# Performance work log

Measured on AMD Instinct MI355X. Metric: run time of the kernel, lower is better.

The kernel has to match this reference:

```python
import jax, jax.numpy as jnp
import numpy as np

B, S, HID, H, DK = 16, 1024, 512, 8, 64
NEG = -1e30


def setup_inputs() -> dict:
    key = jax.random.key(0)
    kx, kl, kq, kk, kv, ko = jax.random.split(key, 6)
    x = jax.random.normal(kx, (B, S, HID), dtype=jnp.float32)
    # mask is a prefix of ones per sample (the torch code fills nmask[i, :nsum, :nsum])
    lengths = jax.random.randint(kl, (B,), S // 2, S + 1)
    mask = (jnp.arange(S)[None, :] < lengths[:, None]).astype(jnp.int32)
    scale = 0.02
    Wq = jax.random.normal(kq, (H, HID, DK), dtype=jnp.float32) * scale  # stacked per-head Linear weights
    Wk = jax.random.normal(kk, (H, HID, DK), dtype=jnp.float32) * scale
    Wv = jax.random.normal(kv, (H, HID, DK), dtype=jnp.float32) * scale
    Wout = jax.random.normal(ko, (H * DK, HID), dtype=jnp.float32) * scale
    return {"x": x, "mask": mask, "Wq": Wq, "Wk": Wk, "Wv": Wv, "Wout": Wout}


def reference(x, mask, Wq, Wk, Wv, Wout):
    # x: [B,S,HID], mask: [B,S] int prefix mask
    nsum = mask.sum(-1).astype(jnp.float32)          # [B]
    valid = mask.astype(bool)                         # [B,S]
    pair = valid[:, :, None] & valid[:, None, :]      # [B,S,S] == nmask from the torch loop
    # batched per-head projections (equivalent to the per-head Linear loop)
    Q = jnp.einsum('bsh,nhd->bnsd', x, Wq)            # [B,H,S,DK]
    K = jnp.einsum('bsh,nhd->bnsd', x, Wk)
    V = jnp.einsum('bsh,nhd->bnsd', x, Wv)
    scores = jnp.einsum('bnqd,bnkd->bnqk', Q, K)      # [B,H,S,S]
    scores = scores / jnp.sqrt(nsum)[:, None, None, None]  # per-sample sqrt(len) scale
    scores = jnp.where(pair[:, None, :, :], scores, NEG)   # masked_softmax: -1e30 at masked slots
    p = jax.nn.softmax(scores, axis=-1)
    attn = jnp.einsum('bnqk,bnkd->bnqd', p, V)        # [B,H,S,DK]
    h = attn.transpose(0, 2, 1, 3).reshape(B, S, H * DK)  # concat heads along feature dim
    return jnp.einsum('bsf,fh->bsh', h, Wout)         # W_out, no bias
```

## Files before the change

kernel.cpp:

```cpp
#include <hip/hip_runtime.h>
#include <math.h>

constexpr int CB = 16;
constexpr int CS = 1024;
constexpr int CHID = 512;
constexpr int CH = 8;
constexpr int CDK = 64;

typedef _Float16 f16;
typedef __attribute__((ext_vector_type(8))) _Float16 f16x8;
typedef __attribute__((ext_vector_type(4))) _Float16 f16x4;
typedef __attribute__((ext_vector_type(4))) float f32x4;

__device__ inline f32x4 mfma16(f16x8 a, f16x8 b, f32x4 c) {
  return __builtin_amdgcn_mfma_f32_16x16x32_f16(a, b, c, 0, 0, 0);
}

__global__ __launch_bounds__(256) void lengths_kernel(const int* __restrict__ mask,
                                                      int* __restrict__ lens) {
  const int b = blockIdx.x, t = threadIdx.x;
  __shared__ int red[256];
  int s = 0;
  for (int i = t; i < CS; i += 256) s += mask[b * CS + i];
  red[t] = s;
  __syncthreads();
  for (int off = 128; off > 0; off >>= 1) {
    if (t < off) red[t] += red[t + off];
    __syncthreads();
  }
  if (t == 0) lens[b] = red[0];
}

__global__ __launch_bounds__(256) void cast_x_kernel(const float4* __restrict__ x,
                                                     f16x4* __restrict__ xh) {
  const int idx = blockIdx.x * 256 + threadIdx.x;
  const float4 v = x[idx];
  f16x4 o;
  o[0] = (f16)v.x; o[1] = (f16)v.y; o[2] = (f16)v.z; o[3] = (f16)v.w;
  xh[idx] = o;
}

__global__ __launch_bounds__(256) void cast_w_kernel(const float* __restrict__ Wq,
                                                     const float* __restrict__ Wk,
                                                     const float* __restrict__ Wv,
                                                     const float* __restrict__ Wout,
                                                     f16* __restrict__ wtAll) {
  const int y = blockIdx.y;
  const int o0 = (blockIdx.x * 256 + threadIdx.x) * 4;
  f16* D = wtAll + (size_t)y * 262144;
  f16x4 d;
  if (y < 3) {
    const float* W = (y == 0) ? Wq : (y == 1) ? Wk : Wv;
    const int h = o0 >> 15, n = (o0 >> 9) & 63, k = o0 & 511;
    const size_t in = (size_t)h * 32768 + (size_t)k * 64 + n;
#pragma unroll
    for (int j = 0; j < 4; ++j) d[j] = (f16)W[in + (size_t)j * 64];
  } else {
    const int n = o0 >> 9, k = o0 & 511;
#pragma unroll
    for (int j = 0; j < 4; ++j) d[j] = (f16)Wout[(size_t)(k + j) * 512 + n];
  }
  *(f16x4*)&D[o0] = d;
}

__global__ __launch_bounds__(256) void qkvf_kernel(
    const f16* __restrict__ xh, const f16* __restrict__ wtAll,
    const int* __restrict__ lens, f16* __restrict__ Qh, f16* __restrict__ Kh,
    f16* __restrict__ Vth) {
  const int rt = blockIdx.x, ct = blockIdx.y;
  const int which = ct >> 2, hp = ct & 3;
  const f16* Wt = wtAll + (size_t)which * 262144 + (size_t)hp * 65536;
  const int row0 = rt * 128;
  const int b = row0 >> 10, s0 = row0 & 1023;
  const int h0 = hp * 2;
  const int t = threadIdx.x;
  const int w = t >> 6, lane = t & 63, quad = lane >> 4, lcol = lane & 15;
  const int wr = w >> 1, wc = w & 1;

  __shared__ union SM {
    struct { f16 Xs[128][40]; f16 Ws[128][40]; } a;
    f16 Ts[128][136];
  } sm;

  f32x4 acc[4][4];
#pragma unroll
  for (int i = 0; i < 4; ++i)
#pragma unroll
    for (int j = 0; j < 4; ++j) acc[i][j] = (f32x4){0.f, 0.f, 0.f, 0.f};

  for (int k0 = 0; k0 < CHID; k0 += 32) {
#pragma unroll
    for (int i = 0; i < 2; ++i) {
      const int c = t + 256 * i, r = c >> 2, sg = c & 3;
      *(f16x8*)&sm.a.Xs[r][sg * 8] =
          *(const f16x8*)&xh[(size_t)(row0 + r) * CHID + k0 + sg * 8];
      *(f16x8*)&sm.a.Ws[r][sg * 8] =
          *(const f16x8*)&Wt[(size_t)r * CHID + k0 + sg * 8];
    }
    __syncthreads();
    f16x8 af[4], bf[4];
#pragma unroll
    for (int i = 0; i < 4; ++i)
      af[i] = *(const f16x8*)&sm.a.Xs[wr * 64 + i * 16 + lcol][quad * 8];
#pragma unroll
    for (int j = 0; j < 4; ++j)
      bf[j] = *(const f16x8*)&sm.a.Ws[wc * 64 + j * 16 + lcol][quad * 8];
#pragma unroll
    for (int i = 0; i < 4; ++i)
#pragma unroll
      for (int j = 0; j < 4; ++j) acc[i][j] = mfma16(af[i], bf[j], acc[i][j]);
    __syncthreads();
  }

  if (which == 2) {
#pragma unroll
    for (int i = 0; i < 4; ++i)
#pragma unroll
      for (int j = 0; j < 4; ++j)
#pragma unroll
        for (int rr = 0; rr < 4; ++rr)
          sm.Ts[wc * 64 + j * 16 + lcol][wr * 64 + i * 16 + quad * 4 + rr] =
              (f16)acc[i][j][rr];
    __syncthreads();
    const int nl = t >> 1, half = t & 1;
    const int h = h0 + (nl >> 6), d = nl & 63;
    f16* dst = &Vth[(((size_t)b * CH + h) * CDK + d) * CS + s0 + half * 64];
#pragma unroll
    for (int c8 = 0; c8 < 8; ++c8)
      *(f16x8*)&dst[c8 * 8] = *(const f16x8*)&sm.Ts[nl][half * 64 + c8 * 8];
  } else {
    f16* O = (which == 0) ? Qh : Kh;
    const float qsc = (which == 0) ? rsqrtf((float)lens[b]) : 1.0f;
    const int h = h0 + wc;
#pragma unroll
    for (int i = 0; i < 4; ++i) {
#pragma unroll
      for (int rr = 0; rr < 4; ++rr) {
        const int s = s0 + wr * 64 + i * 16 + quad * 4 + rr;
        const size_t base = (((size_t)b * CH + h) * CS + s) * CDK;
#pragma unroll
        for (int j = 0; j < 4; ++j)
          O[base + j * 16 + lcol] = (f16)(acc[i][j][rr] * qsc);
      }
    }
  }
}

__global__ __launch_bounds__(256) void vsum_kernel(const f16* __restrict__ Vth,
                                                   float* __restrict__ Vsum) {
  const int bh = blockIdx.x;
  const int t = threadIdx.x;
  const int r = t >> 2, c = t & 3;
  const f16* src = Vth + ((size_t)bh * CDK + r) * CS;
  float s = 0.f;
  for (int i = 0; i < CS; i += 32) {
    f16x8 v = *(const f16x8*)&src[i + c * 8];
#pragma unroll
    for (int j = 0; j < 8; ++j) s += (float)v[j];
  }
  s += __shfl_xor(s, 1);
  s += __shfl_xor(s, 2);
  if (c == 0) Vsum[(size_t)bh * CDK + r] = s;
}

__global__ __launch_bounds__(256) void attn_kernel(
    const f16* __restrict__ Qh, const f16* __restrict__ Kh,
    const f16* __restrict__ Vth, const int* __restrict__ lens,
    const float* __restrict__ Vsum, f16* __restrict__ Hbh) {
  const int qt = blockIdx.x, h = blockIdx.y, b = blockIdx.z;
  const int n = lens[b];
  const int nt = (n + 63) >> 6;
  const int t = threadIdx.x, w = t >> 6, lane = t & 63, quad = lane >> 4,
            lcol = lane & 15;

  __shared__ f16 Ks[64][72];
  __shared__ f16 Vs[64][72];
  __shared__ f16 Pt[4][32][72];

  const size_t bh = ((size_t)b * CH + h) * CS;
  const size_t bhd = ((size_t)b * CH + h) * CDK;

  const int qbase = qt * 128 + w * 32;
  f16x8 qa[2][2];
#pragma unroll
  for (int set = 0; set < 2; ++set) {
    const size_t qr = bh + qbase + set * 16 + lcol;
    qa[set][0] = *(const f16x8*)&Qh[qr * CDK + quad * 8];
    qa[set][1] = *(const f16x8*)&Qh[qr * CDK + 32 + quad * 8];
  }

  f32x4 o[2][4];
#pragma unroll
  for (int set = 0; set < 2; ++set)
#pragma unroll
    for (int dt = 0; dt < 4; ++dt) o[set][dt] = (f32x4){0.f, 0.f, 0.f, 0.f};
  float lp[2][4] = {{0.f, 0.f, 0.f, 0.f}, {0.f, 0.f, 0.f, 0.f}};

  for (int kt = 0; kt < nt; ++kt) {
    __syncthreads();
#pragma unroll
    for (int i = 0; i < 2; ++i) {
      const int c = t + 256 * i, r = c >> 3, sg = c & 7;
      *(f16x8*)&Ks[r][sg * 8] =
          *(const f16x8*)&Kh[(bh + kt * 64 + r) * CDK + sg * 8];
      *(f16x8*)&Vs[r][sg * 8] =
          *(const f16x8*)&Vth[(bhd + r) * CS + kt * 64 + sg * 8];
    }
    __syncthreads();

#pragma unroll
    for (int set = 0; set < 2; ++set) {
      f32x4 st[4];
#pragma unroll
      for (int ct = 0; ct < 4; ++ct) {
        const f16x8 kb0 = *(const f16x8*)&Ks[ct * 16 + lcol][quad * 8];
        const f16x8 kb1 = *(const f16x8*)&Ks[ct * 16 + lcol][32 + quad * 8];
        st[ct] = mfma16(qa[set][0], kb0, (f32x4){0.f, 0.f, 0.f, 0.f});
        st[ct] = mfma16(qa[set][1], kb1, st[ct]);
      }
#pragma unroll
      for (int ct = 0; ct < 4; ++ct) {
        const bool kvld = (kt * 64 + ct * 16 + lcol) < n;
#pragma unroll
        for (int r = 0; r < 4; ++r) {
          float p = __expf(st[ct][r]);
          p = kvld ? p : 0.f;
          lp[set][r] += p;
          Pt[w][set * 16 + quad * 4 + r][ct * 16 + lcol] = (f16)p;
        }
      }
    }

    f16x8 pa[2][2];
#pragma unroll
    for (int set = 0; set < 2; ++set) {
      pa[set][0] = *(const f16x8*)&Pt[w][set * 16 + lcol][quad * 8];
      pa[set][1] = *(const f16x8*)&Pt[w][set * 16 + lcol][32 + quad * 8];
    }

#pragma unroll
    for (int dt = 0; dt < 4; ++dt) {
      const f16x8 vb0 = *(const f16x8*)&Vs[dt * 16 + lcol][quad * 8];
      const f16x8 vb1 = *(const f16x8*)&Vs[dt * 16 + lcol][32 + quad * 8];
#pragma unroll
      for (int set = 0; set < 2; ++set) {
        o[set][dt] = mfma16(pa[set][0], vb0, o[set][dt]);
        o[set][dt] = mfma16(pa[set][1], vb1, o[set][dt]);
      }
    }
  }

  float invl[2][4];
#pragma unroll
  for (int set = 0; set < 2; ++set)
#pragma unroll
    for (int r = 0; r < 4; ++r) {
      float v = lp[set][r];
      v += __shfl_xor(v, 1);
      v += __shfl_xor(v, 2);
      v += __shfl_xor(v, 4);
      v += __shfl_xor(v, 8);
      invl[set][r] = 1.0f / v;
    }

#pragma unroll
  for (int set = 0; set < 2; ++set)
#pragma unroll
    for (int dt = 0; dt < 4; ++dt)
#pragma unroll
      for (int r = 0; r < 4; ++r) {
        const int srow = qbase + set * 16 + quad * 4 + r;
        const int d = dt * 16 + lcol;
        const float val = (srow < n) ? o[set][dt][r] * invl[set][r]
                                     : Vsum[bhd + d] * (1.0f / 1024.0f);
        Hbh[((size_t)b * CS + srow) * (CH * CDK) + h * CDK + d] = (f16)val;
      }
}

__global__ __launch_bounds__(256) void outp_kernel(const f16* __restrict__ Hbh,
                                                   const f16* __restrict__ woutt,
                                                   float* __restrict__ out) {
  const int rt = blockIdx.x, ctile = blockIdx.y;
  const int row0 = rt * 128, col0 = ctile * 128;
  const f16* Wt = woutt + (size_t)col0 * CHID;
  const int t = threadIdx.x;
  const int w = t >> 6, lane = t & 63, quad = lane >> 4, lcol = lane & 15;
  const int wr = w >> 1, wc = w & 1;

  __shared__ f16 Hs[128][40];
  __shared__ f16 Ws[128][40];

  f32x4 acc[4][4];
#pragma unroll
  for (int i = 0; i < 4; ++i)
#pragma unroll
    for (int j = 0; j < 4; ++j) acc[i][j] = (f32x4){0.f, 0.f, 0.f, 0.f};

  for (int k0 = 0; k0 < CHID; k0 += 32) {
#pragma unroll
    for (int i = 0; i < 2; ++i) {
      const int c = t + 256 * i, r = c >> 2, sg = c & 3;
      *(f16x8*)&Hs[r][sg * 8] =
          *(const f16x8*)&Hbh[(size_t)(row0 + r) * CHID + k0 + sg * 8];
      *(f16x8*)&Ws[r][sg * 8] =
          *(const f16x8*)&Wt[(size_t)r * CHID + k0 + sg * 8];
    }
    __syncthreads();
    f16x8 af[4], bf[4];
#pragma unroll
    for (int i = 0; i < 4; ++i)
      af[i] = *(const f16x8*)&Hs[wr * 64 + i * 16 + lcol][quad * 8];
#pragma unroll
    for (int j = 0; j < 4; ++j)
      bf[j] = *(const f16x8*)&Ws[wc * 64 + j * 16 + lcol][quad * 8];
#pragma unroll
    for (int i = 0; i < 4; ++i)
#pragma unroll
      for (int j = 0; j < 4; ++j) acc[i][j] = mfma16(af[i], bf[j], acc[i][j]);
    __syncthreads();
  }

#pragma unroll
  for (int i = 0; i < 4; ++i) {
#pragma unroll
    for (int rr = 0; rr < 4; ++rr) {
      const size_t rg = row0 + wr * 64 + i * 16 + quad * 4 + rr;
#pragma unroll
      for (int j = 0; j < 4; ++j)
        out[rg * CHID + col0 + wc * 64 + j * 16 + lcol] = acc[i][j][rr];
    }
  }
}

extern "C" void kernel_launch(void* const* d_in, const int* in_sizes, int n_in,
                              void* d_out, int out_size, void* d_ws,
                              size_t ws_size, hipStream_t stream) {
  const float* x = (const float*)d_in[0];
  const int* mask = (const int*)d_in[1];
  const float* Wq = (const float*)d_in[2];
  const float* Wk = (const float*)d_in[3];
  const float* Wv = (const float*)d_in[4];
  const float* Wout = (const float*)d_in[5];
  float* out = (float*)d_out;

  char* ws = (char*)d_ws;
  int* lens = (int*)ws;
  size_t off = 1024;
  const size_t NX = (size_t)CB * CS * CHID;
  const size_t NW = (size_t)CH * CHID * CDK;
  f16* xh = (f16*)(ws + off);    off += NX * 2;
  f16* wtAll = (f16*)(ws + off); off += NW * 4 * 2;
  f16* Qh = (f16*)(ws + off);    off += NX * 2;
  f16* Kh = (f16*)(ws + off);    off += NX * 2;
  f16* Vth = (f16*)(ws + off);   off += NX * 2;
  f16* Hbh = (f16*)(ws + off);   off += NX * 2;
  float* Vsum = (float*)(ws + off); off += (size_t)CB * CH * CDK * 4;
  f16* woutt = wtAll + NW * 3;

  lengths_kernel<<<CB, 256, 0, stream>>>(mask, lens);
  cast_x_kernel<<<NX / 4 / 256, 256, 0, stream>>>((const float4*)x, (f16x4*)xh);
  cast_w_kernel<<<dim3(256, 4), 256, 0, stream>>>(Wq, Wk, Wv, Wout, wtAll);
  qkvf_kernel<<<dim3(128, 12), 256, 0, stream>>>(xh, wtAll, lens, Qh, Kh, Vth);
  vsum_kernel<<<CB * CH, 256, 0, stream>>>(Vth, Vsum);
  attn_kernel<<<dim3(CS / 128, CH, CB), 256, 0, stream>>>(Qh, Kh, Vth, lens,
                                                          Vsum, Hbh);
  outp_kernel<<<dim3(128, 4), 256, 0, stream>>>(Hbh, woutt, out);
}
```

Baseline: 222.2 us.

## Prefetch tiles in registers, fuse V column sums, transpose weights via LDS

Adds register double-buffering to the QKV projection, attention and output GEMM loops so the next tile's global loads are in flight while MFMAs run on the current tile. Drops the separate vsum kernel and instead accumulates per-feature V sums in the QKV epilogue with atomicAdd, zeroing Vsum in the lengths kernel. Rewrites the weight cast/transpose to go through shared memory for coalesced reads. In exchange it uses more registers, and the float atomics make the V-sum accumulation order nondeterministic.

```diff
diff --git a/kernel.cpp b/kernel.cpp
--- a/kernel.cpp
+++ b/kernel.cpp
@@ -17,8 +17,12 @@
 }
 
 __global__ __launch_bounds__(256) void lengths_kernel(const int* __restrict__ mask,
-                                                      int* __restrict__ lens) {
+                                                      int* __restrict__ lens,
+                                                      float* __restrict__ Vsum) {
   const int b = blockIdx.x, t = threadIdx.x;
+  const int g = b * 256 + t;
+  Vsum[g * 2] = 0.f;
+  Vsum[g * 2 + 1] = 0.f;
   __shared__ int red[256];
   int s = 0;
   for (int i = t; i < CS; i += 256) s += mask[b * CS + i];
@@ -45,28 +49,55 @@
                                                      const float* __restrict__ Wv,
                                                      const float* __restrict__ Wout,
                                                      f16* __restrict__ wtAll) {
-  const int y = blockIdx.y;
-  const int o0 = (blockIdx.x * 256 + threadIdx.x) * 4;
-  f16* D = wtAll + (size_t)y * 262144;
-  f16x4 d;
-  if (y < 3) {
-    const float* W = (y == 0) ? Wq : (y == 1) ? Wk : Wv;
-    const int h = o0 >> 15, n = (o0 >> 9) & 63, k = o0 & 511;
-    const size_t in = (size_t)h * 32768 + (size_t)k * 64 + n;
-#pragma unroll
-    for (int j = 0; j < 4; ++j) d[j] = (f16)W[in + (size_t)j * 64];
+  const int y = blockIdx.y, kb = blockIdx.x, t = threadIdx.x;
+  const int k0 = kb * 64;
+  const float* src;
+  int ldsrc;
+  f16* dst;
+  if (y < 24) {
+    const int which = y >> 3, h = y & 7;
+    const float* W = (which == 0) ? Wq : (which == 1) ? Wk : Wv;
+    src = W + (size_t)h * 32768 + (size_t)k0 * 64;
+    ldsrc = 64;
+    dst = wtAll + (size_t)which * 262144 + (size_t)h * 32768;
   } else {
-    const int n = o0 >> 9, k = o0 & 511;
-#pragma unroll
-    for (int j = 0; j < 4; ++j) d[j] = (f16)Wout[(size_t)(k + j) * 512 + n];
-  }
-  *(f16x4*)&D[o0] = d;
+    const int c = y - 24;
+    src = Wout + (size_t)k0 * 512 + c * 64;
+    ldsrc = 512;
+    dst = wtAll + (size_t)3 * 262144 + (size_t)c * 64 * 512;
+  }
+
+  __shared__ float Ts[64][68];
+  {
+    const int kr = t >> 4, cg = (t & 15) * 4;
+#pragma unroll
+    for (int rr = 0; rr < 4; ++rr) {
+      const float4 v = *(const float4*)&src[(size_t)(rr * 16 + kr) * ldsrc + cg];
+      Ts[rr * 16 + kr][cg] = v.x;
+      Ts[rr * 16 + kr][cg + 1] = v.y;
+      Ts[rr * 16 + kr][cg + 2] = v.z;
+      Ts[rr * 16 + kr][cg + 3] = v.w;
+    }
+  }
+  __syncthreads();
+  {
+    const int n = t >> 2, seg = t & 3;
+    f16x8 a, b;
+#pragma unroll
+    for (int j = 0; j < 8; ++j) {
+      a[j] = (f16)Ts[seg * 16 + j][n];
+      b[j] = (f16)Ts[seg * 16 + 8 + j][n];
+    }
+    f16* d = &dst[(size_t)n * 512 + k0 + seg * 16];
+    *(f16x8*)d = a;
+    *(f16x8*)(d + 8) = b;
+  }
 }
 
 __global__ __launch_bounds__(256) void qkvf_kernel(
     const f16* __restrict__ xh, const f16* __restrict__ wtAll,
     const int* __restrict__ lens, f16* __restrict__ Qh, f16* __restrict__ Kh,
-    f16* __restrict__ Vth) {
+    f16* __restrict__ Vth, float* __restrict__ Vsum) {
   const int rt = blockIdx.x, ct = blockIdx.y;
   const int which = ct >> 2, hp = ct & 3;
   const f16* Wt = wtAll + (size_t)which * 262144 + (size_t)hp * 65536;
@@ -88,16 +119,30 @@
 #pragma unroll
     for (int j = 0; j < 4; ++j) acc[i][j] = (f32x4){0.f, 0.f, 0.f, 0.f};
 
+  f16x8 px[2], pw[2];
+#pragma unroll
+  for (int i = 0; i < 2; ++i) {
+    const int c = t + 256 * i, r = c >> 2, sg = c & 3;
+    px[i] = *(const f16x8*)&xh[(size_t)(row0 + r) * CHID + sg * 8];
+    pw[i] = *(const f16x8*)&Wt[(size_t)r * CHID + sg * 8];
+  }
+
   for (int k0 = 0; k0 < CHID; k0 += 32) {
+    __syncthreads();
 #pragma unroll
     for (int i = 0; i < 2; ++i) {
       const int c = t + 256 * i, r = c >> 2, sg = c & 3;
-      *(f16x8*)&sm.a.Xs[r][sg * 8] =
-          *(const f16x8*)&xh[(size_t)(row0 + r) * CHID + k0 + sg * 8];
-      *(f16x8*)&sm.a.Ws[r][sg * 8] =
-          *(const f16x8*)&Wt[(size_t)r * CHID + k0 + sg * 8];
-    }
-    __syncthreads();
+      *(f16x8*)&sm.a.Xs[r][sg * 8] = px[i];
+      *(f16x8*)&sm.a.Ws[r][sg * 8] = pw[i];
+    }
+    __syncthreads();
+    const int kn = (k0 + 32 < CHID) ? k0 + 32 : k0;
+#pragma unroll
+    for (int i = 0; i < 2; ++i) {
+      const int c = t + 256 * i, r = c >> 2, sg = c & 3;
+      px[i] = *(const f16x8*)&xh[(size_t)(row0 + r) * CHID + kn + sg * 8];
+      pw[i] = *(const f16x8*)&Wt[(size_t)r * CHID + kn + sg * 8];
+    }
     f16x8 af[4], bf[4];
 #pragma unroll
     for (int i = 0; i < 4; ++i)
@@ -109,10 +154,25 @@
     for (int i = 0; i < 4; ++i)
 #pragma unroll
       for (int j = 0; j < 4; ++j) acc[i][j] = mfma16(af[i], bf[j], acc[i][j]);
-    __syncthreads();
   }
 
   if (which == 2) {
+#pragma unroll
+    for (int j = 0; j < 4; ++j) {
+      float ps = 0.f;
+#pragma unroll
+      for (int i = 0; i < 4; ++i)
+#pragma unroll
+        for (int rr = 0; rr < 4; ++rr) ps += acc[i][j][rr];
+      ps += __shfl_xor(ps, 16);
+      ps += __shfl_xor(ps, 32);
+      if (quad == 0) {
+        const int d128 = wc * 64 + j * 16 + lcol;
+        const int h = h0 + (d128 >> 6), d = d128 & 63;
+        atomicAdd(&Vsum[((size_t)b * CH + h) * CDK + d], ps);
+      }
+    }
+    __syncthreads();
 #pragma unroll
     for (int i = 0; i < 4; ++i)
 #pragma unroll
@@ -144,23 +204,6 @@
       }
     }
   }
-}
-
-__global__ __launch_bounds__(256) void vsum_kernel(const f16* __restrict__ Vth,
-                                                   float* __restrict__ Vsum) {
-  const int bh = blockIdx.x;
-  const int t = threadIdx.x;
-  const int r = t >> 2, c = t & 3;
-  const f16* src = Vth + ((size_t)bh * CDK + r) * CS;
-  float s = 0.f;
-  for (int i = 0; i < CS; i += 32) {
-    f16x8 v = *(const f16x8*)&src[i + c * 8];
-#pragma unroll
-    for (int j = 0; j < 8; ++j) s += (float)v[j];
-  }
-  s += __shfl_xor(s, 1);
-  s += __shfl_xor(s, 2);
-  if (c == 0) Vsum[(size_t)bh * CDK + r] = s;
 }
 
 __global__ __launch_bounds__(256) void attn_kernel(
@@ -196,17 +239,30 @@
     for (int dt = 0; dt < 4; ++dt) o[set][dt] = (f32x4){0.f, 0.f, 0.f, 0.f};
   float lp[2][4] = {{0.f, 0.f, 0.f, 0.f}, {0.f, 0.f, 0.f, 0.f}};
 
+  f16x8 pk[2], pv[2];
+#pragma unroll
+  for (int i = 0; i < 2; ++i) {
+    const int c = t + 256 * i, r = c >> 3, sg = c & 7;
+    pk[i] = *(const f16x8*)&Kh[(bh + r) * CDK + sg * 8];
+    pv[i] = *(const f16x8*)&Vth[(bhd + r) * CS + sg * 8];
+  }
+
   for (int kt = 0; kt < nt; ++kt) {
     __syncthreads();
 #pragma unroll
     for (int i = 0; i < 2; ++i) {
       const int c = t + 256 * i, r = c >> 3, sg = c & 7;
-      *(f16x8*)&Ks[r][sg * 8] =
-          *(const f16x8*)&Kh[(bh + kt * 64 + r) * CDK + sg * 8];
-      *(f16x8*)&Vs[r][sg * 8] =
-          *(const f16x8*)&Vth[(bhd + r) * CS + kt * 64 + sg * 8];
-    }
-    __syncthreads();
+      *(f16x8*)&Ks[r][sg * 8] = pk[i];
+      *(f16x8*)&Vs[r][sg * 8] = pv[i];
+    }
+    __syncthreads();
+    const int ktn = (kt + 1 < nt) ? kt + 1 : kt;
+#pragma unroll
+    for (int i = 0; i < 2; ++i) {
+      const int c = t + 256 * i, r = c >> 3, sg = c & 7;
+      pk[i] = *(const f16x8*)&Kh[(bh + ktn * 64 + r) * CDK + sg * 8];
+      pv[i] = *(const f16x8*)&Vth[(bhd + r) * CS + ktn * 64 + sg * 8];
+    }
 
 #pragma unroll
     for (int set = 0; set < 2; ++set) {
@@ -296,16 +352,30 @@
 #pragma unroll
     for (int j = 0; j < 4; ++j) acc[i][j] = (f32x4){0.f, 0.f, 0.f, 0.f};
 
+  f16x8 ph[2], pw[2];
+#pragma unroll
+  for (int i = 0; i < 2; ++i) {
+    const int c = t + 256 * i, r = c >> 2, sg = c & 3;
+    ph[i] = *(const f16x8*)&Hbh[(size_t)(row0 + r) * CHID + sg * 8];
+    pw[i] = *(const f16x8*)&Wt[(size_t)r * CHID + sg * 8];
+  }
+
   for (int k0 = 0; k0 < CHID; k0 += 32) {
+    __syncthreads();
 #pragma unroll
     for (int i = 0; i < 2; ++i) {
       const int c = t + 256 * i, r = c >> 2, sg = c & 3;
-      *(f16x8*)&Hs[r][sg * 8] =
-          *(const f16x8*)&Hbh[(size_t)(row0 + r) * CHID + k0 + sg * 8];
-      *(f16x8*)&Ws[r][sg * 8] =
-          *(const f16x8*)&Wt[(size_t)r * CHID + k0 + sg * 8];
-    }
-    __syncthreads();
+      *(f16x8*)&Hs[r][sg * 8] = ph[i];
+      *(f16x8*)&Ws[r][sg * 8] = pw[i];
+    }
+    __syncthreads();
+    const int kn = (k0 + 32 < CHID) ? k0 + 32 : k0;
+#pragma unroll
+    for (int i = 0; i < 2; ++i) {
+      const int c = t + 256 * i, r = c >> 2, sg = c & 3;
+      ph[i] = *(const f16x8*)&Hbh[(size_t)(row0 + r) * CHID + kn + sg * 8];
+      pw[i] = *(const f16x8*)&Wt[(size_t)r * CHID + kn + sg * 8];
+    }
     f16x8 af[4], bf[4];
 #pragma unroll
     for (int i = 0; i < 4; ++i)
@@ -317,7 +387,6 @@
     for (int i = 0; i < 4; ++i)
 #pragma unroll
       for (int j = 0; j < 4; ++j) acc[i][j] = mfma16(af[i], bf[j], acc[i][j]);
-    __syncthreads();
   }
 
 #pragma unroll
@@ -357,11 +426,11 @@
   float* Vsum = (float*)(ws + off); off += (size_t)CB * CH * CDK * 4;
   f16* woutt = wtAll + NW * 3;
 
-  lengths_kernel<<<CB, 256, 0, stream>>>(mask, lens);
+  lengths_kernel<<<CB, 256, 0, stream>>>(mask, lens, Vsum);
   cast_x_kernel<<<NX / 4 / 256, 256, 0, stream>>>((const float4*)x, (f16x4*)xh);
-  cast_w_kernel<<<dim3(256, 4), 256, 0, stream>>>(Wq, Wk, Wv, Wout, wtAll);
-  qkvf_kernel<<<dim3(128, 12), 256, 0, stream>>>(xh, wtAll, lens, Qh, Kh, Vth);
-  vsum_kernel<<<CB * CH, 256, 0, stream>>>(Vth, Vsum);
+  cast_w_kernel<<<dim3(8, 32), 256, 0, stream>>>(Wq, Wk, Wv, Wout, wtAll);
+  qkvf_kernel<<<dim3(128, 12), 256, 0, stream>>>(xh, wtAll, lens, Qh, Kh, Vth,
+                                                 Vsum);
   attn_kernel<<<dim3(CS / 128, CH, CB), 256, 0, stream>>>(Qh, Kh, Vth, lens,
                                                           Vsum, Hbh);
   outp_kernel<<<dim3(128, 4), 256, 0, stream>>>(Hbh, woutt, out);
```

Result: faster. 213.5 us (-3.9%).
